# Optimization experiments

Measured on AMD Instinct MI355X. Metric: run time of the kernel, lower is better.

The kernel has to match this reference:

```python
import jax, jax.numpy as jnp
import numpy as np

EMBED = 1024
NHEAD = 16
HEAD_DIM = EMBED // NHEAD
DFF = 4096
TOP_K = 64
LN_EPS = 1e-5


def _layernorm(x, g, b):
    mu = jnp.mean(x, axis=-1, keepdims=True)
    var = jnp.var(x, axis=-1, keepdims=True)
    return (x - mu) * jax.lax.rsqrt(var + LN_EPS) * g + b


def setup_inputs() -> dict:
    key = jax.random.key(0)
    ks = jax.random.split(key, 12)
    s = 0.02
    return {
        "x": jax.random.normal(ks[0], (2, 2048, EMBED), dtype=jnp.float32),
        "Wq": jax.random.normal(ks[1], (EMBED, EMBED), dtype=jnp.float32) * s,
        "bq": jnp.zeros((EMBED,), jnp.float32),
        "Wk": jax.random.normal(ks[2], (EMBED, EMBED), dtype=jnp.float32) * s,
        "bk": jnp.zeros((EMBED,), jnp.float32),
        "Wv": jax.random.normal(ks[3], (EMBED, EMBED), dtype=jnp.float32) * s,
        "bv": jnp.zeros((EMBED,), jnp.float32),
        "Wo": jax.random.normal(ks[4], (EMBED, EMBED), dtype=jnp.float32) * s,
        "bo": jnp.zeros((EMBED,), jnp.float32),
        "g1": jnp.ones((EMBED,), jnp.float32),
        "be1": jnp.zeros((EMBED,), jnp.float32),
        "g2": jnp.ones((EMBED,), jnp.float32),
        "be2": jnp.zeros((EMBED,), jnp.float32),
        "W1": jax.random.normal(ks[5], (EMBED, DFF), dtype=jnp.float32) * s,
        "b1": jnp.zeros((DFF,), jnp.float32),
        "W2": jax.random.normal(ks[6], (DFF, EMBED), dtype=jnp.float32) * s,
        "b2": jnp.zeros((EMBED,), jnp.float32),
    }


def reference(x, Wq, bq, Wk, bk, Wv, bv, Wo, bo, g1, be1, g2, be2, W1, b1, W2, b2):
    B, N, E = x.shape
    res = x
    h = _layernorm(x, g1, be1)
    # [B, H, N, D]
    q = (h @ Wq + bq).reshape(B, N, NHEAD, HEAD_DIM).transpose(0, 2, 1, 3)
    k = (h @ Wk + bk).reshape(B, N, NHEAD, HEAD_DIM).transpose(0, 2, 1, 3)
    v = (h @ Wv + bv).reshape(B, N, NHEAD, HEAD_DIM).transpose(0, 2, 1, 3)
    scores = jnp.einsum("bhqd,bhkd->bhqk", q, k) / jnp.sqrt(jnp.float32(HEAD_DIM))
    if TOP_K < N:
        topv, _ = jax.lax.top_k(scores, TOP_K)  # [B,H,N,TOP_K]
        thresh = topv[..., -1:, ]
        scores = jnp.where(scores < thresh, -jnp.inf, scores)
    attn = jax.nn.softmax(scores, axis=-1)
    out = jnp.einsum("bhqk,bhkd->bhqd", attn, v)
    out = out.transpose(0, 2, 1, 3).reshape(B, N, E)
    out = out @ Wo + bo
    x1 = res + out  # dropout is identity at eval
    h2 = _layernorm(x1, g2, be2)
    ff = jax.nn.gelu(h2 @ W1 + b1, approximate=False) @ W2 + b2
    return x1 + ff
```

## Files before the change

### kernel.cpp

```cpp
#include <hip/hip_runtime.h>

typedef short short8v __attribute__((ext_vector_type(8)));
typedef float floatx4 __attribute__((ext_vector_type(4)));
typedef unsigned short us4 __attribute__((ext_vector_type(4)));
typedef unsigned short us2 __attribute__((ext_vector_type(2)));

#define EMB 1024
#define QKVW 3072
#define SEQ 2048
#define NH 16
#define HD 64
#define TOPK 64
#define QBLK 16
#define CAP 128
#define SROW 2056
#define QSCALE 0.18033688f
#define ATTN_SMEM (QBLK * SROW * 2 + QBLK * CAP * 4)

#define GLDS16(gp, lp)                                                        \
  __builtin_amdgcn_global_load_lds(                                           \
      (const __attribute__((address_space(1))) void*)(gp),                    \
      (__attribute__((address_space(3))) void*)(lp), 16, 0, 0)

#if __has_builtin(__builtin_amdgcn_exp2f)
#define EXP2F(x) __builtin_amdgcn_exp2f(x)
#else
#define EXP2F(x) exp2f(x)
#endif

static __device__ __forceinline__ unsigned short f2b(float f) {
  union { float f; unsigned u; } in; in.f = f;
  unsigned u = in.u;
  return (unsigned short)((u + 0x7FFFu + ((u >> 16) & 1u)) >> 16);
}
static __device__ __forceinline__ float b2f(unsigned short b) {
  union { unsigned u; float f; } o; o.u = ((unsigned)b) << 16;
  return o.f;
}
static __device__ __forceinline__ unsigned mmap(unsigned s) {
  return (s & 0x8000u) ? (~s & 0xFFFFu) : (s | 0x8000u);
}
static __device__ __forceinline__ unsigned short munmap(unsigned u) {
  return (u & 0x8000u) ? (unsigned short)(u ^ 0x8000u) : (unsigned short)(~u & 0xFFFFu);
}
static __device__ __forceinline__ unsigned mmap2(unsigned s) {
  const unsigned t = ((s >> 15) & 0x00010001u) * 0x7FFFu;
  return s ^ (0x80008000u | t);
}

__global__ __launch_bounds__(256) void ln_kernel(const float* __restrict__ X,
    const float* __restrict__ gam, const float* __restrict__ bet,
    unsigned short* __restrict__ H) {
  const int row = blockIdx.x;
  const int tid = threadIdx.x;
  const float4 v = *(const float4*)&X[(size_t)row * EMB + tid * 4];
  float s1 = v.x + v.y + v.z + v.w;
  float s2 = v.x * v.x + v.y * v.y + v.z * v.z + v.w * v.w;
#pragma unroll
  for (int off = 32; off; off >>= 1) { s1 += __shfl_xor(s1, off); s2 += __shfl_xor(s2, off); }
  __shared__ float red[2][4];
  const int w = tid >> 6, l = tid & 63;
  if (l == 0) { red[0][w] = s1; red[1][w] = s2; }
  __syncthreads();
  s1 = red[0][0] + red[0][1] + red[0][2] + red[0][3];
  s2 = red[1][0] + red[1][1] + red[1][2] + red[1][3];
  const float mu = s1 * (1.f / EMB);
  const float var = s2 * (1.f / EMB) - mu * mu;
  const float rs = rsqrtf(var + 1e-5f);
  const float4 gv = *(const float4*)&gam[tid * 4];
  const float4 bv = *(const float4*)&bet[tid * 4];
  us4 o;
  o.x = f2b((v.x - mu) * rs * gv.x + bv.x);
  o.y = f2b((v.y - mu) * rs * gv.y + bv.y);
  o.z = f2b((v.z - mu) * rs * gv.z + bv.z);
  o.w = f2b((v.w - mu) * rs * gv.w + bv.w);
  *(us4*)&H[(size_t)row * EMB + tid * 4] = o;
}

__global__ __launch_bounds__(256) void wcvt_all_kernel(
    const float* __restrict__ Wq, const float* __restrict__ Wk,
    const float* __restrict__ Wv, const float* __restrict__ Wo,
    const float* __restrict__ W1, const float* __restrict__ W2,
    const float* __restrict__ bq, const float* __restrict__ bk,
    const float* __restrict__ bv,
    unsigned short* __restrict__ WqkvT, unsigned short* __restrict__ WoT,
    unsigned short* __restrict__ W1T, unsigned short* __restrict__ W2T,
    float* __restrict__ bqkv) {
  const int bid = blockIdx.x;
  const int tid = threadIdx.x;
  if (bid >= 3072) {
    const int i = (bid - 3072) * 256 + tid;
    float v;
    if (i < 1024) v = bq[i] * QSCALE;
    else if (i < 2048) v = bk[i - 1024];
    else v = bv[i - 2048];
    bqkv[i] = v;
    return;
  }
  const float* W; unsigned short* WT; int K, N, t; float scale = 1.f;
  if (bid < 768) {
    const int seg = bid >> 8; t = bid & 255;
    W = (seg == 0) ? Wq : ((seg == 1) ? Wk : Wv);
    WT = WqkvT + (size_t)seg * 1024 * 1024;
    K = 1024; N = 1024;
    if (seg == 0) scale = QSCALE;
  } else if (bid < 1024) {
    t = bid - 768;  W = Wo; WT = WoT; K = 1024; N = 1024;
  } else if (bid < 2048) {
    t = bid - 1024; W = W1; WT = W1T; K = 1024; N = 4096;
  } else {
    t = bid - 2048; W = W2; WT = W2T; K = 4096; N = 1024;
  }
  const int sh = (N == 4096) ? 6 : 4;
  const int n0 = (t & ((1 << sh) - 1)) * 64, k0 = (t >> sh) * 64;
  __shared__ unsigned short tl[64][72];
#pragma unroll
  for (int i = 0; i < 4; ++i) {
    const int f = i * 256 + tid;
    const int k = f >> 4, n4 = (f & 15) * 4;
    const float4 v = *(const float4*)&W[(size_t)(k0 + k) * N + n0 + n4];
    tl[n4 + 0][k] = f2b(v.x * scale);
    tl[n4 + 1][k] = f2b(v.y * scale);
    tl[n4 + 2][k] = f2b(v.z * scale);
    tl[n4 + 3][k] = f2b(v.w * scale);
  }
  __syncthreads();
#pragma unroll
  for (int i = 0; i < 2; ++i) {
    const int f = i * 256 + tid;
    const int n = f >> 3, c8 = (f & 7) * 8;
    short8v o;
#pragma unroll
    for (int j = 0; j < 8; ++j) o[j] = (short)tl[n][c8 + j];
    *(short8v*)&WT[(size_t)(n0 + n) * K + k0 + c8] = o;
  }
}

static __device__ __forceinline__ void xcd_tile(int& bm, int& bn, int tn) {
  const int gx = gridDim.x;
  const int nwg = gx * gridDim.y;
  const int flat = blockIdx.y * gx + blockIdx.x;
  const int q8 = nwg >> 3;
  const int wg = (flat & 7) * q8 + (flat >> 3);
  bm = (wg / gx) * 128;
  bn = (wg % gx) * tn;
}

template <int EPI>
__global__ __launch_bounds__(256) void gemm_bt4_kernel(
    const unsigned short* __restrict__ A, const unsigned short* __restrict__ BT,
    const float* __restrict__ bias, const float* __restrict__ res,
    void* __restrict__ Cout, int M, int N, int K) {
  __shared__ __align__(16) unsigned short lA[128 * 64];
  __shared__ __align__(16) unsigned short lB[128 * 64];
  const int tid = threadIdx.x;
  const int l = tid & 63, w = tid >> 6;
  const int wm = (w >> 1) * 64, wn = (w & 1) * 64;
  int bm, bn; xcd_tile(bm, bn, 128);
  const int g = l >> 4, r16 = l & 15;
  const int lr8 = l >> 3;
  const int lc8s = (((l & 7) ^ (lr8 & 7)) * 8);
  const int xr = (r16 & 7) * 8;
  floatx4 acc[4][4] = {};
  for (int kt = 0; kt < K; kt += 64) {
#pragma unroll
    for (int j = 0; j < 4; ++j) {
      GLDS16(&A[(size_t)(bm + w * 32 + j * 8 + lr8) * K + kt + lc8s],
             &lA[(w * 32 + j * 8) * 64]);
      GLDS16(&BT[(size_t)(bn + w * 32 + j * 8 + lr8) * K + kt + lc8s],
             &lB[(w * 32 + j * 8) * 64]);
    }
    __syncthreads();
#pragma unroll
    for (int kk = 0; kk < 2; ++kk) {
      short8v a[4], b[4];
      const int co = (kk * 32 + g * 8) ^ xr;
#pragma unroll
      for (int m = 0; m < 4; ++m) a[m] = *(const short8v*)&lA[(wm + m * 16 + r16) * 64 + co];
#pragma unroll
      for (int n = 0; n < 4; ++n) b[n] = *(const short8v*)&lB[(wn + n * 16 + r16) * 64 + co];
#pragma unroll
      for (int m = 0; m < 4; ++m)
#pragma unroll
        for (int n = 0; n < 4; ++n)
          acc[m][n] = __builtin_amdgcn_mfma_f32_16x16x32_bf16(a[m], b[n], acc[m][n], 0, 0, 0);
    }
    __syncthreads();
  }
#pragma unroll
  for (int m = 0; m < 4; ++m) {
#pragma unroll
    for (int n = 0; n < 4; ++n) {
#pragma unroll
      for (int r = 0; r < 4; ++r) {
        const int gm = bm + wm + m * 16 + g * 4 + r;
        const int gn = bn + wn + n * 16 + r16;
        float v = acc[m][n][r] + bias[gn];
        if constexpr (EPI == 0) {
          ((unsigned short*)Cout)[(size_t)gm * N + gn] = f2b(v);
        } else if constexpr (EPI == 1) {
          const float ge = 0.5f * v * (1.f + erff(v * 0.70710678118f));
          ((unsigned short*)Cout)[(size_t)gm * N + gn] = f2b(ge);
        } else {
          ((float*)Cout)[(size_t)gm * N + gn] = v + res[(size_t)gm * N + gn];
        }
      }
    }
  }
}

template <int EPI>
__global__ __launch_bounds__(256) void gemm_n64_kernel(
    const unsigned short* __restrict__ A, const unsigned short* __restrict__ BT,
    const float* __restrict__ bias, const float* __restrict__ res,
    void* __restrict__ Cout, int M, int N, int K) {
  __shared__ __align__(16) unsigned short lA[128 * 32];
  __shared__ __align__(16) unsigned short lB[64 * 32];
  const int tid = threadIdx.x;
  const int l = tid & 63, w = tid >> 6;
  const int wm = (w & 1) * 64, wn = (w >> 1) * 32;
  int bm, bn; xcd_tile(bm, bn, 64);
  const int g = l >> 4, r16 = l & 15;
  const int lr = l >> 2, lc = (l & 3) * 8;
  floatx4 acc[4][2] = {};
  for (int kt = 0; kt < K; kt += 32) {
#pragma unroll
    for (int j = 0; j < 2; ++j)
      GLDS16(&A[(size_t)(bm + w * 32 + j * 16 + lr) * K + kt + lc],
             &lA[(w * 32 + j * 16) * 32]);
    GLDS16(&BT[(size_t)(bn + w * 16 + lr) * K + kt + lc], &lB[(w * 16) * 32]);
    __syncthreads();
    short8v a[4], b[2];
#pragma unroll
    for (int m = 0; m < 4; ++m) a[m] = *(const short8v*)&lA[(wm + m * 16 + r16) * 32 + g * 8];
#pragma unroll
    for (int n = 0; n < 2; ++n) b[n] = *(const short8v*)&lB[(wn + n * 16 + r16) * 32 + g * 8];
#pragma unroll
    for (int m = 0; m < 4; ++m)
#pragma unroll
      for (int n = 0; n < 2; ++n)
        acc[m][n] = __builtin_amdgcn_mfma_f32_16x16x32_bf16(a[m], b[n], acc[m][n], 0, 0, 0);
    __syncthreads();
  }
#pragma unroll
  for (int m = 0; m < 4; ++m) {
#pragma unroll
    for (int n = 0; n < 2; ++n) {
#pragma unroll
      for (int r = 0; r < 4; ++r) {
        const int gm = bm + wm + m * 16 + g * 4 + r;
        const int gn = bn + wn + n * 16 + r16;
        float v = acc[m][n][r] + bias[gn];
        if constexpr (EPI == 0) {
          ((unsigned short*)Cout)[(size_t)gm * N + gn] = f2b(v);
        } else if constexpr (EPI == 1) {
          const float ge = 0.5f * v * (1.f + erff(v * 0.70710678118f));
          ((unsigned short*)Cout)[(size_t)gm * N + gn] = f2b(ge);
        } else {
          ((float*)Cout)[(size_t)gm * N + gn] = v + res[(size_t)gm * N + gn];
        }
      }
    }
  }
}

__global__ __launch_bounds__(1024, 8) void attn_kernel(
    const unsigned short* __restrict__ qkv, unsigned short* __restrict__ O) {
  extern __shared__ unsigned short smem[];
  unsigned short (*scores)[SROW] = (unsigned short(*)[SROW])smem;
  unsigned* hist = (unsigned*)(smem + QBLK * SROW);

  const int tid = threadIdx.x;
  const int l = tid & 63, w = tid >> 6;
  const int g = l >> 4, r16 = l & 15;
  const int qb = blockIdx.x;
  const int h = blockIdx.y;
  const int bz = blockIdx.z;
  const size_t rowbase = (size_t)bz * SEQ;
  const int hcol = h * HD;

  ((uint2*)hist)[tid] = uint2{0u, 0u};

  {
    const size_t qrow = (rowbase + qb * QBLK + r16) * QKVW + hcol;
    const short8v qf0 = *(const short8v*)&qkv[qrow + g * 8];
    const short8v qf1 = *(const short8v*)&qkv[qrow + 32 + g * 8];
    const int kbase = w * 128;
#pragma unroll 2
    for (int kti = 0; kti < 8; ++kti) {
      const int key0 = kbase + kti * 16;
      const size_t krow = (rowbase + key0 + r16) * QKVW + 1024 + hcol;
      const short8v kf0 = *(const short8v*)&qkv[krow + g * 8];
      const short8v kf1 = *(const short8v*)&qkv[krow + 32 + g * 8];
      floatx4 acc = {0.f, 0.f, 0.f, 0.f};
      acc = __builtin_amdgcn_mfma_f32_16x16x32_bf16(kf0, qf0, acc, 0, 0, 0);
      acc = __builtin_amdgcn_mfma_f32_16x16x32_bf16(kf1, qf1, acc, 0, 0, 0);
      union { float f; unsigned u; } c0, c1, c2, c3;
      c0.f = acc[0]; c1.f = acc[1]; c2.f = acc[2]; c3.f = acc[3];
      const unsigned p01 = __builtin_amdgcn_perm(c1.u, c0.u, 0x07060302u);
      const unsigned p23 = __builtin_amdgcn_perm(c3.u, c2.u, 0x07060302u);
      uint2 pw; pw.x = mmap2(p01); pw.y = mmap2(p23);
      *(uint2*)&scores[r16][key0 + g * 4] = pw;
    }
  }
  __syncthreads();

  const unsigned long long ltmask = (1ull << l) - 1ull;
  const int quarter = l >> 4, j16 = l & 15;
  const int q = w;
  unsigned* srow32 = (unsigned*)&scores[q][0];
  unsigned* comp = &hist[q * CAP];

  unsigned ux[16];
  us2 mx2 = {0, 0};
#pragma unroll
  for (int i = 0; i < 16; ++i) {
    const unsigned x = srow32[l + 64 * i];
    ux[i] = x;
    union { unsigned u; us2 v; } c; c.u = x;
    mx2 = __builtin_elementwise_max(mx2, c.v);
  }
  unsigned um = (mx2.x > mx2.y) ? (unsigned)mx2.x : (unsigned)mx2.y;
#pragma unroll
  for (int off = 32; off; off >>= 1) {
    const unsigned o2 = (unsigned)__shfl_xor((int)um, off);
    um = (o2 > um) ? o2 : um;
  }
  const float mf = b2f(munmap(um));

#pragma unroll
  for (int i = 0; i < 16; ++i) {
    const unsigned d0 = um - (ux[i] & 0xFFFFu);
    const unsigned d1 = um - (ux[i] >> 16);
    if (d0 < 256u) atomicAdd(&comp[d0 >> 1], 1u << ((d0 & 1u) * 16));
    if (d1 < 256u) atomicAdd(&comp[d1 >> 1], 1u << ((d1 & 1u) * 16));
  }
  asm volatile("s_waitcnt lgkmcnt(0)" ::: "memory");
  unsigned ut;
  {
    const unsigned w0 = comp[2 * l], w1 = comp[2 * l + 1];
    const unsigned c0 = w0 & 0xFFFFu, c1 = w0 >> 16, c2 = w1 & 0xFFFFu, c3 = w1 >> 16;
    const unsigned s4 = c0 + c1 + c2 + c3;
    unsigned incl = s4;
#pragma unroll
    for (int off = 1; off < 64; off <<= 1) {
      const unsigned t2 = (unsigned)__shfl_up((int)incl, off);
      if (l >= off) incl += t2;
    }
    const unsigned pre = incl - s4;
    unsigned dc = 0xFFFFFFFFu;
    if      (pre + c0 >= TOPK)           dc = 4 * l;
    else if (pre + c0 + c1 >= TOPK)      dc = 4 * l + 1;
    else if (pre + c0 + c1 + c2 >= TOPK) dc = 4 * l + 2;
    else if (incl >= TOPK)               dc = 4 * l + 3;
#pragma unroll
    for (int off = 32; off; off >>= 1) {
      const unsigned o2 = (unsigned)__shfl_xor((int)dc, off);
      dc = (o2 < dc) ? o2 : dc;
    }
    if (dc != 0xFFFFFFFFu) {
      ut = um - dc;
    } else {
      unsigned t = 0;
#pragma unroll 1
      for (int bit = 15; bit >= 0; --bit) {
        const unsigned cand = t | (1u << bit);
        int c = 0;
#pragma unroll
        for (int i = 0; i < 16; ++i) {
          c += __popcll(__ballot((ux[i] & 0xFFFFu) >= cand));
          c += __popcll(__ballot((ux[i] >> 16) >= cand));
        }
        if (c >= TOPK) t = cand;
      }
      ut = t;
    }
  }

  unsigned base = 0;
#pragma unroll
  for (int i = 0; i < 16; ++i) {
    const unsigned u0 = ux[i] & 0xFFFFu, u1 = ux[i] >> 16;
    const bool k0 = (u0 >= ut), k1 = (u1 >= ut);
    const unsigned key0 = 2 * (l + 64 * i);
    const unsigned long long m0 = __ballot(k0);
    if (k0) {
      const unsigned pos = base + (unsigned)__popcll(m0 & ltmask);
      if (pos < CAP) comp[pos] = (key0 << 16) | u0;
    }
    base += (unsigned)__popcll(m0);
    const unsigned long long m1 = __ballot(k1);
    if (k1) {
      const unsigned pos = base + (unsigned)__popcll(m1 & ltmask);
      if (pos < CAP) comp[pos] = ((key0 + 1) << 16) | u1;
    }
    base += (unsigned)__popcll(m1);
  }
  const unsigned cnt = (base < CAP) ? base : CAP;

  float e0 = 0.f, e1 = 0.f;
  unsigned c0v = 0, c1v = 0;
  const bool h0 = ((unsigned)l < cnt), h1 = ((unsigned)(l + 64) < cnt);
  if (h0) {
    c0v = comp[l];
    e0 = EXP2F(b2f(munmap(c0v & 0xFFFFu)) - mf);
  }
  if (h1) {
    c1v = comp[l + 64];
    e1 = EXP2F(b2f(munmap(c1v & 0xFFFFu)) - mf);
  }
  float lsum = e0 + e1;
#pragma unroll
  for (int off = 32; off; off >>= 1) lsum += __shfl_xor(lsum, off);
  const float rinv = 1.f / lsum;
  if (h0) {
    unsigned pp; asm("v_cvt_pk_bf16_f32 %0, %1, %2" : "=v"(pp) : "v"(e0), "v"(e0));
    comp[l] = (c0v & 0xFFFF0000u) | (pp & 0xFFFFu);
  }
  if (h1) {
    unsigned pp; asm("v_cvt_pk_bf16_f32 %0, %1, %2" : "=v"(pp) : "v"(e1), "v"(e1));
    comp[l + 64] = (c1v & 0xFFFF0000u) | (pp & 0xFFFFu);
  }

  const unsigned short* vbase = &qkv[rowbase * QKVW + 2048 + hcol + j16 * 4];
  float a0 = 0.f, a1 = 0.f, a2 = 0.f, a3 = 0.f;
#pragma unroll 4
  for (int k = 0; k < 16; ++k) {
    const unsigned c = comp[k * 4 + quarter];
    const float p = b2f((unsigned short)(c & 0xFFFFu));
    const unsigned idx = c >> 16;
    const uint2 vv = *(const uint2*)&vbase[(size_t)idx * QKVW];
    union { unsigned u; float f; } t0, t1, t2, t3;
    t0.u = vv.x << 16; t1.u = vv.x & 0xFFFF0000u;
    t2.u = vv.y << 16; t3.u = vv.y & 0xFFFF0000u;
    a0 += p * t0.f; a1 += p * t1.f; a2 += p * t2.f; a3 += p * t3.f;
  }
#pragma unroll 1
  for (unsigned k = 64; k < cnt; k += 4) {
    const unsigned kk = k + quarter;
    const unsigned c = (kk < cnt) ? comp[kk] : 0u;
    const float p = b2f((unsigned short)(c & 0xFFFFu));
    const unsigned idx = c >> 16;
    const uint2 vv = *(const uint2*)&vbase[(size_t)idx * QKVW];
    union { unsigned u; float f; } t0, t1, t2, t3;
    t0.u = vv.x << 16; t1.u = vv.x & 0xFFFF0000u;
    t2.u = vv.y << 16; t3.u = vv.y & 0xFFFF0000u;
    a0 += p * t0.f; a1 += p * t1.f; a2 += p * t2.f; a3 += p * t3.f;
  }
  a0 += __shfl_xor(a0, 16); a0 += __shfl_xor(a0, 32);
  a1 += __shfl_xor(a1, 16); a1 += __shfl_xor(a1, 32);
  a2 += __shfl_xor(a2, 16); a2 += __shfl_xor(a2, 32);
  a3 += __shfl_xor(a3, 16); a3 += __shfl_xor(a3, 32);
  if (l < 16) {
    unsigned w0, w1;
    const float r0 = a0 * rinv, r1 = a1 * rinv, r2 = a2 * rinv, r3 = a3 * rinv;
    asm("v_cvt_pk_bf16_f32 %0, %1, %2" : "=v"(w0) : "v"(r0), "v"(r1));
    asm("v_cvt_pk_bf16_f32 %0, %1, %2" : "=v"(w1) : "v"(r2), "v"(r3));
    uint2 ow; ow.x = w0; ow.y = w1;
    *(uint2*)&O[(rowbase + qb * QBLK + q) * EMB + hcol + j16 * 4] = ow;
  }
}

extern "C" void kernel_launch(void* const* d_in, const int* in_sizes, int n_in,
                              void* d_out, int out_size, void* d_ws, size_t ws_size,
                              hipStream_t stream) {
  (void)in_sizes; (void)n_in; (void)out_size; (void)ws_size;
  const float* x  = (const float*)d_in[0];
  const float* Wq = (const float*)d_in[1];
  const float* bq = (const float*)d_in[2];
  const float* Wk = (const float*)d_in[3];
  const float* bk = (const float*)d_in[4];
  const float* Wv = (const float*)d_in[5];
  const float* bv = (const float*)d_in[6];
  const float* Wo = (const float*)d_in[7];
  const float* bo = (const float*)d_in[8];
  const float* g1 = (const float*)d_in[9];
  const float* be1 = (const float*)d_in[10];
  const float* g2 = (const float*)d_in[11];
  const float* be2 = (const float*)d_in[12];
  const float* W1 = (const float*)d_in[13];
  const float* b1 = (const float*)d_in[14];
  const float* W2 = (const float*)d_in[15];
  const float* b2 = (const float*)d_in[16];
  float* out = (float*)d_out;

  char* ws = (char*)d_ws;
  float* x1 = (float*)ws;
  unsigned short* hbuf  = (unsigned short*)(ws + ((size_t)16 << 20));
  unsigned short* qkvb  = (unsigned short*)(ws + ((size_t)24 << 20));
  unsigned short* Ob    = (unsigned short*)(ws + ((size_t)48 << 20));
  unsigned short* ff1   = (unsigned short*)(ws + ((size_t)24 << 20));
  float* bqkv           = (float*)(ws + ((size_t)48 << 20));
  unsigned short* WqkvT = (unsigned short*)(ws + ((size_t)56 << 20));
  unsigned short* WoT   = (unsigned short*)(ws + ((size_t)62 << 20));
  unsigned short* W1T   = (unsigned short*)(ws + ((size_t)64 << 20));
  unsigned short* W2T   = (unsigned short*)(ws + ((size_t)72 << 20));

  wcvt_all_kernel<<<dim3(3084), 256, 0, stream>>>(Wq, Wk, Wv, Wo, W1, W2, bq, bk, bv,
                                                  WqkvT, WoT, W1T, W2T, bqkv);

  ln_kernel<<<dim3(4096), 256, 0, stream>>>(x, g1, be1, hbuf);
  gemm_bt4_kernel<0><<<dim3(24, 32), 256, 0, stream>>>(hbuf, WqkvT, bqkv, nullptr, qkvb,
                                                       4096, QKVW, 1024);
  (void)hipFuncSetAttribute((const void*)attn_kernel,
                            hipFuncAttributeMaxDynamicSharedMemorySize, ATTN_SMEM);
  attn_kernel<<<dim3(128, 16, 2), 1024, ATTN_SMEM, stream>>>(qkvb, Ob);
  gemm_n64_kernel<2><<<dim3(16, 32), 256, 0, stream>>>(Ob, WoT, bo, x, x1, 4096, 1024, 1024);
  ln_kernel<<<dim3(4096), 256, 0, stream>>>(x1, g2, be2, hbuf);
  gemm_bt4_kernel<1><<<dim3(32, 32), 256, 0, stream>>>(hbuf, W1T, b1, nullptr, ff1,
                                                       4096, 4096, 1024);
  gemm_n64_kernel<2><<<dim3(16, 32), 256, 0, stream>>>(ff1, W2T, b2, x1, out, 4096, 1024, 4096);
}
```

Baseline: 398.4 us.

## Double-buffer GEMM LDS tiles and use LDS atomics for top-k compaction

Both GEMM kernels now double-buffer their LDS tiles, prefetching the next K-slice with global_load_lds while MFMAs consume the current one. The bt4 kernel drops from a 64-wide K tile with an XOR swizzle to a 32-wide unswizzled tile, which doubles the number of loop iterations and barriers and may add LDS bank conflicts. Separately, the attention top-k compaction replaces ballot/popcount prefix sums with per-row LDS atomicAdd counters, so the order of kept entries is no longer deterministic. There is also only one barrier per iteration protecting buffer reuse, which looks correct because the prefetch targets the other buffer.

New measurement: 391.3 us. About the same (-1.8%).

```diff
diff --git a/kernel.cpp b/kernel.cpp
--- a/kernel.cpp
+++ b/kernel.cpp
@@ -15,7 +15,7 @@
 #define CAP 128
 #define SROW 2056
 #define QSCALE 0.18033688f
-#define ATTN_SMEM (QBLK * SROW * 2 + QBLK * CAP * 4)
+#define ATTN_SMEM (QBLK * SROW * 2 + QBLK * CAP * 4 + 64)
 
 #define GLDS16(gp, lp)                                                        \
   __builtin_amdgcn_global_load_lds(                                           \
@@ -151,41 +151,48 @@
     const unsigned short* __restrict__ A, const unsigned short* __restrict__ BT,
     const float* __restrict__ bias, const float* __restrict__ res,
     void* __restrict__ Cout, int M, int N, int K) {
-  __shared__ __align__(16) unsigned short lA[128 * 64];
-  __shared__ __align__(16) unsigned short lB[128 * 64];
+  __shared__ __align__(16) unsigned short lA[2][128 * 32];
+  __shared__ __align__(16) unsigned short lB[2][128 * 32];
   const int tid = threadIdx.x;
   const int l = tid & 63, w = tid >> 6;
   const int wm = (w >> 1) * 64, wn = (w & 1) * 64;
   int bm, bn; xcd_tile(bm, bn, 128);
   const int g = l >> 4, r16 = l & 15;
-  const int lr8 = l >> 3;
-  const int lc8s = (((l & 7) ^ (lr8 & 7)) * 8);
-  const int xr = (r16 & 7) * 8;
+  const int lr = l >> 2, lc = (l & 3) * 8;
   floatx4 acc[4][4] = {};
-  for (int kt = 0; kt < K; kt += 64) {
-#pragma unroll
-    for (int j = 0; j < 4; ++j) {
-      GLDS16(&A[(size_t)(bm + w * 32 + j * 8 + lr8) * K + kt + lc8s],
-             &lA[(w * 32 + j * 8) * 64]);
-      GLDS16(&BT[(size_t)(bn + w * 32 + j * 8 + lr8) * K + kt + lc8s],
-             &lB[(w * 32 + j * 8) * 64]);
-    }
+  const int nt = K >> 5;
+#pragma unroll
+  for (int j = 0; j < 2; ++j) {
+    GLDS16(&A[(size_t)(bm + w * 32 + j * 16 + lr) * K + lc], &lA[0][(w * 32 + j * 16) * 32]);
+    GLDS16(&BT[(size_t)(bn + w * 32 + j * 16 + lr) * K + lc], &lB[0][(w * 32 + j * 16) * 32]);
+  }
+  __syncthreads();
+  int cur = 0;
+  for (int t = 0; t < nt; ++t) {
+    if (t + 1 < nt) {
+      const int kt = (t + 1) << 5;
+#pragma unroll
+      for (int j = 0; j < 2; ++j) {
+        GLDS16(&A[(size_t)(bm + w * 32 + j * 16 + lr) * K + kt + lc],
+               &lA[cur ^ 1][(w * 32 + j * 16) * 32]);
+        GLDS16(&BT[(size_t)(bn + w * 32 + j * 16 + lr) * K + kt + lc],
+               &lB[cur ^ 1][(w * 32 + j * 16) * 32]);
+      }
+    }
+    short8v a[4], b[4];
+#pragma unroll
+    for (int m = 0; m < 4; ++m)
+      a[m] = *(const short8v*)&lA[cur][(wm + m * 16 + r16) * 32 + g * 8];
+#pragma unroll
+    for (int n = 0; n < 4; ++n)
+      b[n] = *(const short8v*)&lB[cur][(wn + n * 16 + r16) * 32 + g * 8];
+#pragma unroll
+    for (int m = 0; m < 4; ++m)
+#pragma unroll
+      for (int n = 0; n < 4; ++n)
+        acc[m][n] = __builtin_amdgcn_mfma_f32_16x16x32_bf16(a[m], b[n], acc[m][n], 0, 0, 0);
     __syncthreads();
-#pragma unroll
-    for (int kk = 0; kk < 2; ++kk) {
-      short8v a[4], b[4];
-      const int co = (kk * 32 + g * 8) ^ xr;
-#pragma unroll
-      for (int m = 0; m < 4; ++m) a[m] = *(const short8v*)&lA[(wm + m * 16 + r16) * 64 + co];
-#pragma unroll
-      for (int n = 0; n < 4; ++n) b[n] = *(const short8v*)&lB[(wn + n * 16 + r16) * 64 + co];
-#pragma unroll
-      for (int m = 0; m < 4; ++m)
-#pragma unroll
-        for (int n = 0; n < 4; ++n)
-          acc[m][n] = __builtin_amdgcn_mfma_f32_16x16x32_bf16(a[m], b[n], acc[m][n], 0, 0, 0);
-    }
-    __syncthreads();
+    cur ^= 1;
   }
 #pragma unroll
   for (int m = 0; m < 4; ++m) {
@@ -214,8 +221,8 @@
     const unsigned short* __restrict__ A, const unsigned short* __restrict__ BT,
     const float* __restrict__ bias, const float* __restrict__ res,
     void* __restrict__ Cout, int M, int N, int K) {
-  __shared__ __align__(16) unsigned short lA[128 * 32];
-  __shared__ __align__(16) unsigned short lB[64 * 32];
+  __shared__ __align__(16) unsigned short lA[2][128 * 32];
+  __shared__ __align__(16) unsigned short lB[2][64 * 32];
   const int tid = threadIdx.x;
   const int l = tid & 63, w = tid >> 6;
   const int wm = (w & 1) * 64, wn = (w >> 1) * 32;
@@ -223,24 +230,36 @@
   const int g = l >> 4, r16 = l & 15;
   const int lr = l >> 2, lc = (l & 3) * 8;
   floatx4 acc[4][2] = {};
-  for (int kt = 0; kt < K; kt += 32) {
-#pragma unroll
-    for (int j = 0; j < 2; ++j)
-      GLDS16(&A[(size_t)(bm + w * 32 + j * 16 + lr) * K + kt + lc],
-             &lA[(w * 32 + j * 16) * 32]);
-    GLDS16(&BT[(size_t)(bn + w * 16 + lr) * K + kt + lc], &lB[(w * 16) * 32]);
-    __syncthreads();
+  const int nt = K >> 5;
+#pragma unroll
+  for (int j = 0; j < 2; ++j)
+    GLDS16(&A[(size_t)(bm + w * 32 + j * 16 + lr) * K + lc], &lA[0][(w * 32 + j * 16) * 32]);
+  GLDS16(&BT[(size_t)(bn + w * 16 + lr) * K + lc], &lB[0][(w * 16) * 32]);
+  __syncthreads();
+  int cur = 0;
+  for (int t = 0; t < nt; ++t) {
+    if (t + 1 < nt) {
+      const int kt = (t + 1) << 5;
+#pragma unroll
+      for (int j = 0; j < 2; ++j)
+        GLDS16(&A[(size_t)(bm + w * 32 + j * 16 + lr) * K + kt + lc],
+               &lA[cur ^ 1][(w * 32 + j * 16) * 32]);
+      GLDS16(&BT[(size_t)(bn + w * 16 + lr) * K + kt + lc], &lB[cur ^ 1][(w * 16) * 32]);
+    }
     short8v a[4], b[2];
 #pragma unroll
-    for (int m = 0; m < 4; ++m) a[m] = *(const short8v*)&lA[(wm + m * 16 + r16) * 32 + g * 8];
-#pragma unroll
-    for (int n = 0; n < 2; ++n) b[n] = *(const short8v*)&lB[(wn + n * 16 + r16) * 32 + g * 8];
+    for (int m = 0; m < 4; ++m)
+      a[m] = *(const short8v*)&lA[cur][(wm + m * 16 + r16) * 32 + g * 8];
+#pragma unroll
+    for (int n = 0; n < 2; ++n)
+      b[n] = *(const short8v*)&lB[cur][(wn + n * 16 + r16) * 32 + g * 8];
 #pragma unroll
     for (int m = 0; m < 4; ++m)
 #pragma unroll
       for (int n = 0; n < 2; ++n)
         acc[m][n] = __builtin_amdgcn_mfma_f32_16x16x32_bf16(a[m], b[n], acc[m][n], 0, 0, 0);
     __syncthreads();
+    cur ^= 1;
   }
 #pragma unroll
   for (int m = 0; m < 4; ++m) {
@@ -269,6 +288,7 @@
   extern __shared__ unsigned short smem[];
   unsigned short (*scores)[SROW] = (unsigned short(*)[SROW])smem;
   unsigned* hist = (unsigned*)(smem + QBLK * SROW);
+  unsigned* cnts = (unsigned*)(smem + QBLK * SROW + 4096);
 
   const int tid = threadIdx.x;
   const int l = tid & 63, w = tid >> 6;
@@ -280,6 +300,7 @@
   const int hcol = h * HD;
 
   ((uint2*)hist)[tid] = uint2{0u, 0u};
+  if (tid < 16) cnts[tid] = 0u;
 
   {
     const size_t qrow = (rowbase + qb * QBLK + r16) * QKVW + hcol;
@@ -305,7 +326,6 @@
   }
   __syncthreads();
 
-  const unsigned long long ltmask = (1ull << l) - 1ull;
   const int quarter = l >> 4, j16 = l & 15;
   const int q = w;
   unsigned* srow32 = (unsigned*)&scores[q][0];
@@ -377,26 +397,23 @@
     }
   }
 
-  unsigned base = 0;
 #pragma unroll
   for (int i = 0; i < 16; ++i) {
     const unsigned u0 = ux[i] & 0xFFFFu, u1 = ux[i] >> 16;
-    const bool k0 = (u0 >= ut), k1 = (u1 >= ut);
     const unsigned key0 = 2 * (l + 64 * i);
-    const unsigned long long m0 = __ballot(k0);
-    if (k0) {
-      const unsigned pos = base + (unsigned)__popcll(m0 & ltmask);
+    if (u0 >= ut) {
+      const unsigned pos = atomicAdd(&cnts[q], 1u);
       if (pos < CAP) comp[pos] = (key0 << 16) | u0;
     }
-    base += (unsigned)__popcll(m0);
-    const unsigned long long m1 = __ballot(k1);
-    if (k1) {
-      const unsigned pos = base + (unsigned)__popcll(m1 & ltmask);
+    if (u1 >= ut) {
+      const unsigned pos = atomicAdd(&cnts[q], 1u);
       if (pos < CAP) comp[pos] = ((key0 + 1) << 16) | u1;
     }
-    base += (unsigned)__popcll(m1);
-  }
-  const unsigned cnt = (base < CAP) ? base : CAP;
+  }
+  asm volatile("s_waitcnt lgkmcnt(0)" ::: "memory");
+  unsigned cnt = cnts[q];
+  asm volatile("s_waitcnt lgkmcnt(0)" ::: "memory");
+  cnt = (cnt < CAP) ? cnt : CAP;
 
   float e0 = 0.f, e1 = 0.f;
   unsigned c0v = 0, c1v = 0;
```
